# Optimization experiments

Hardware: AMD Instinct MI355X
Metric: run time of the kernel (lower is better)

The kernel has to match this reference:

```python
import jax, jax.numpy as jnp
import numpy as np

N_NODES = 100000
N_EDGES = 1600000


def setup_inputs() -> dict:
    key = jax.random.key(0)
    ks = jax.random.split(key, 8)
    x = jax.random.normal(ks[0], (N_NODES, 100), dtype=jnp.float32)
    edge_index = jax.random.randint(ks[1], (2, N_EDGES), 0, N_NODES, dtype=jnp.int64)
    edge_weight = jax.random.uniform(ks[2], (N_EDGES,), dtype=jnp.float32)
    # params (kaiming-ish scale)
    W_conv = jax.random.normal(ks[3], (100, 32), dtype=jnp.float32) * (1.0 / np.sqrt(100))
    b_conv = jnp.zeros((32,), jnp.float32)
    W1 = jax.random.normal(ks[4], (32, 16), dtype=jnp.float32) * (1.0 / np.sqrt(32))
    b1 = jnp.zeros((16,), jnp.float32)
    W2 = jax.random.normal(ks[5], (16, 8), dtype=jnp.float32) * (1.0 / np.sqrt(16))
    b2 = jnp.zeros((8,), jnp.float32)
    W3 = jax.random.normal(ks[6], (8, 10), dtype=jnp.float32) * (1.0 / np.sqrt(8))
    b3 = jnp.zeros((10,), jnp.float32)
    return {"x": x, "edge_index": edge_index, "edge_weight": edge_weight,
            "W_conv": W_conv, "b_conv": b_conv, "W1": W1, "b1": b1,
            "W2": W2, "b2": b2, "W3": W3, "b3": b3}


def gcn_conv(x, edge_index, W, b, n_nodes):
    # PyG GCNConv: add self-loops, symmetric deg^-0.5 normalization, unit edge weights
    loop = jnp.arange(n_nodes, dtype=edge_index.dtype)
    src = jnp.concatenate([edge_index[0], loop])
    dst = jnp.concatenate([edge_index[1], loop])
    deg = jax.ops.segment_sum(jnp.ones_like(dst, dtype=x.dtype), dst,
                              num_segments=n_nodes)
    dinv = jax.lax.rsqrt(jnp.maximum(deg, 1e-12))  # deg >= 1 due to self-loops
    norm = dinv[src] * dinv[dst]                   # [E+N]
    h = x @ W                                      # [N, 32]
    msg = h[src] * norm[:, None]                   # gather + scale
    out = jax.ops.segment_sum(msg, dst, num_segments=n_nodes)  # scatter-add
    return out + b


def reference(x, edge_index, edge_weight, W_conv, b_conv, W1, b1, W2, b2, W3, b3):
    # edge_weight is accepted by the original forward but never used (conv1(x, edge_index))
    n_nodes = x.shape[0]
    h = jax.nn.relu(gcn_conv(x, edge_index, W_conv, b_conv, n_nodes))
    # F.dropout with training=False (eval) is identity
    h = jax.nn.relu(h @ W1 + b1)
    h = jax.nn.relu(h @ W2 + b2)
    h = h @ W3 + b3
    return jax.nn.log_softmax(h, axis=1)
```

## Files before the change

### kernel.cpp

```cpp
#include <hip/hip_runtime.h>
#include <hip/hip_fp16.h>
#include <math.h>

#define N_NODES 100000
#define N_EDGES 1600000
#define F_IN 100
#define F_H 32

#define BKT_SHIFT 7
#define BKT_C 128
#define NBK 782
#define BKT_CAP 2560

#define BF_B 1024
#define BF_EPT 8
#define BF_TILE 8192
#define BF_GRID 196

#define XW_ROWS 256
#define XW_S2 51
#define XW_NT 391

#define FUSE_GRID 512
#define SM_BYTES 58624

#define AG_B 512
#define AG_CAP BKT_CAP
#define AG_EPT 5

__global__ __launch_bounds__(BF_B) void fused1_kernel(
        const int* __restrict__ src, const int* __restrict__ dst,
        int* __restrict__ gcursor, int* __restrict__ xwctr,
        unsigned* __restrict__ packed,
        const float* __restrict__ x, const float* __restrict__ W,
        float* __restrict__ h2f) {
    __shared__ char smraw[SM_BYTES] __attribute__((aligned(16)));
    __shared__ int stile;
    int t = threadIdx.x;
    if (blockIdx.x < BF_GRID) {
        int* cnt = (int*)smraw;
        int* lbase = cnt + NBK;
        int* gbase = lbase + NBK;
        int* wsums = gbase + NBK;
        int* ptot = wsums + 16;
        unsigned* stage = (unsigned*)(ptot + 1);
        unsigned short* stageB = (unsigned short*)(stage + BF_TILE);
        long base = (long)blockIdx.x * BF_TILE;
        for (int i = t; i < NBK; i += BF_B) cnt[i] = 0;
        __syncthreads();
        int myb[BF_EPT]; int mypos[BF_EPT]; unsigned mypk[BF_EPT];
#pragma unroll
        for (int k = 0; k < BF_EPT; k++) {
            long e = base + t + (long)k * BF_B;
            myb[k] = -1;
            if (e < N_EDGES) {
                int d = dst[e];
                int sI = src[e];
                int b = d >> BKT_SHIFT;
                myb[k] = b;
                mypk[k] = (unsigned)sI | ((unsigned)(d & (BKT_C - 1)) << 17);
                mypos[k] = atomicAdd(&cnt[b], 1);
            }
        }
        __syncthreads();
        if (t < NBK && cnt[t] > 0)
            gbase[t] = t * BKT_CAP + atomicAdd(&gcursor[t], cnt[t]);
        int lane = t & 63, w = t >> 6;
        int v = (t < NBK) ? cnt[t] : 0;
        int sc = v;
#pragma unroll
        for (int off = 1; off < 64; off <<= 1) {
            int xx = __shfl_up(sc, off, 64);
            if (lane >= off) sc += xx;
        }
        if (lane == 63) wsums[w] = sc;
        __syncthreads();
        int pre = 0;
#pragma unroll
        for (int u = 0; u < 16; u++) pre += (u < w) ? wsums[u] : 0;
        int incl = sc + pre;
        if (t < NBK) lbase[t] = incl - v;
        if (t == BF_B - 1) ptot[0] = incl;
        __syncthreads();
#pragma unroll
        for (int k = 0; k < BF_EPT; k++) {
            if (myb[k] >= 0) {
                int p = lbase[myb[k]] + mypos[k];
                stage[p] = mypk[k];
                stageB[p] = (unsigned short)myb[k];
            }
        }
        __syncthreads();
        int T = ptot[0];
        for (int i = t; i < T; i += BF_B) {
            int b = stageB[i];
            packed[gbase[b] + (i - lbase[b])] = stage[i];
        }
    }
    __half2* xs = (__half2*)smraw;
    for (;;) {
        if (t == 0) stile = atomicAdd(xwctr, 1);
        __syncthreads();
        int tb = stile;
        if (tb >= XW_NT) break;
        int rbase = tb * XW_ROWS;
        int rows = min(XW_ROWS, N_NODES - rbase);
        int total = rows * F_IN;
        const float4* gx4 = (const float4*)(x + (long)rbase * F_IN);
        for (int i4 = t; i4 < (total >> 2); i4 += BF_B) {
            float4 v = gx4[i4];
            int i = i4 << 2;
            int r = i / F_IN;
            int k = i - r * F_IN;
            __half2* p = xs + r * XW_S2 + (k >> 1);
            p[0] = __floats2half2_rn(v.x, v.y);
            p[1] = __floats2half2_rn(v.z, v.w);
        }
        __syncthreads();
        int r = t & (XW_ROWS - 1);
        int colbase = __builtin_amdgcn_readfirstlane((t >> 8) << 3);
        if (r < rows) {
            const float* Wp = W + colbase;
            float acc[8];
#pragma unroll
            for (int j = 0; j < 8; j++) acc[j] = 0.f;
            const __half2* xr = xs + r * XW_S2;
#pragma unroll 5
            for (int k2 = 0; k2 < F_IN / 2; k2++) {
                float2 xv = __half22float2(xr[k2]);
#pragma unroll
                for (int j = 0; j < 8; j++)
                    acc[j] = fmaf(xv.y, Wp[(2 * k2 + 1) * F_H + j],
                                  fmaf(xv.x, Wp[(2 * k2) * F_H + j], acc[j]));
            }
            float4* dst4 = (float4*)(h2f + (long)(rbase + r) * F_H + colbase);
            dst4[0] = make_float4(acc[0], acc[1], acc[2], acc[3]);
            dst4[1] = make_float4(acc[4], acc[5], acc[6], acc[7]);
        }
        __syncthreads();
    }
}

__global__ __launch_bounds__(256) void scale_kernel(
        const int* __restrict__ blen, const unsigned* __restrict__ packed,
        const float* __restrict__ h2f, __half* __restrict__ h2) {
    __shared__ int cnt[BKT_C];
    __shared__ float sdv[BKT_C];
    int t = threadIdx.x;
    int b = blockIdx.x;
    if (t < BKT_C) cnt[t] = 0;
    __syncthreads();
    int beg = b * BKT_CAP, end = beg + blen[b];
    for (int i = beg + t; i < end; i += 256)
        atomicAdd(&cnt[(packed[i] >> 17) & (BKT_C - 1)], 1);
    __syncthreads();
    if (t < BKT_C) sdv[t] = rsqrtf((float)cnt[t] + 1.0f);
    __syncthreads();
    int rbase = b << BKT_SHIFT;
    int rows = min(BKT_C, N_NODES - rbase);
    const float4* src4 = (const float4*)(h2f + (long)rbase * F_H);
    float2* dst2 = (float2*)h2;
    for (int i4 = t; i4 < rows * 8; i4 += 256) {
        float4 v = src4[i4];
        float dv = sdv[i4 >> 3];
        float2 o;
        __half2* oh = (__half2*)&o;
        oh[0] = __floats2half2_rn(v.x * dv, v.y * dv);
        oh[1] = __floats2half2_rn(v.z * dv, v.w * dv);
        dst2[(long)rbase * 8 + i4] = o;
    }
}

__global__ __launch_bounds__(AG_B) void agg_kernel(
        const int* __restrict__ blen, const unsigned* __restrict__ packed,
        const __half* __restrict__ h2,
        const float* __restrict__ bc,
        const float* __restrict__ W1, const float* __restrict__ b1,
        const float* __restrict__ W2, const float* __restrict__ b2,
        const float* __restrict__ W3, const float* __restrict__ b3,
        float* __restrict__ out) {
    __shared__ float accL[BKT_C * 33];
    __shared__ int esrc[AG_CAP];
    __shared__ int cnt[BKT_C];
    __shared__ int lbase[BKT_C];
    __shared__ int wsum;
    __shared__ float sbc[32], sW1[512], sb1[16], sW2[128], sb2[8], sW3[80], sb3[10];
    int t = threadIdx.x;
    if (t < 32) sbc[t] = bc[t];
    if (t < 512) sW1[t] = W1[t];
    if (t < 16) sb1[t] = b1[t];
    if (t < 128) sW2[t] = W2[t];
    if (t < 8) sb2[t] = b2[t];
    if (t < 80) sW3[t] = W3[t];
    if (t < 10) sb3[t] = b3[t];

    int b = blockIdx.x;
    int beg = b * BKT_CAP;
    int cnum = blen[b];
    if (t < BKT_C) cnt[t] = 0;
    __syncthreads();
    unsigned pk[AG_EPT]; int pos[AG_EPT];
#pragma unroll
    for (int k = 0; k < AG_EPT; k++) {
        int idx = t + k * AG_B;
        pk[k] = 0xFFFFFFFFu;
        if (idx < cnum) {
            unsigned p = packed[beg + idx];
            pk[k] = p;
            pos[k] = atomicAdd(&cnt[(p >> 17) & (BKT_C - 1)], 1);
        }
    }
    __syncthreads();
    {
        int lane = t & 63;
        int v = 0;
        if (t < BKT_C) {
            v = cnt[t];
#pragma unroll
            for (int off = 1; off < 64; off <<= 1) {
                int xx = __shfl_up(v, off, 64);
                if (lane >= off) v += xx;
            }
            if (t == 63) wsum = v;
        }
        __syncthreads();
        if (t < BKT_C) {
            if (t >= 64) v += wsum;
            lbase[t] = v;
        }
    }
    __syncthreads();
#pragma unroll
    for (int k = 0; k < AG_EPT; k++) {
        if (pk[k] != 0xFFFFFFFFu) {
            int lid = (pk[k] >> 17) & (BKT_C - 1);
            esrc[lbase[lid] - cnt[lid] + pos[k]] = (int)(pk[k] & 0x1FFFF);
        }
    }
    __syncthreads();
    {
        int g = t >> 2, l = t & 3;
        const float4* h2o = (const float4*)h2;
        int e = lbase[g] - cnt[g];
        int eend = lbase[g];
        float a0 = 0.f, a1 = 0.f, a2 = 0.f, a3 = 0.f;
        float a4 = 0.f, a5 = 0.f, a6 = 0.f, a7 = 0.f;
        for (; e + 8 <= eend; e += 8) {
            int s0 = esrc[e], s1 = esrc[e+1], s2 = esrc[e+2], s3 = esrc[e+3];
            int s4 = esrc[e+4], s5 = esrc[e+5], s6 = esrc[e+6], s7 = esrc[e+7];
            float4 q0 = h2o[s0 * 4 + l];
            float4 q1 = h2o[s1 * 4 + l];
            float4 q2 = h2o[s2 * 4 + l];
            float4 q3 = h2o[s3 * 4 + l];
            float4 q4 = h2o[s4 * 4 + l];
            float4 q5 = h2o[s5 * 4 + l];
            float4 q6 = h2o[s6 * 4 + l];
            float4 q7 = h2o[s7 * 4 + l];
#pragma unroll
            for (int u = 0; u < 8; u++) {
                float4 q = (u == 0) ? q0 : (u == 1) ? q1 : (u == 2) ? q2 :
                           (u == 3) ? q3 : (u == 4) ? q4 : (u == 5) ? q5 :
                           (u == 6) ? q6 : q7;
                const __half2* hp = (const __half2*)&q;
                float2 f0 = __half22float2(hp[0]);
                float2 f1 = __half22float2(hp[1]);
                float2 f2 = __half22float2(hp[2]);
                float2 f3 = __half22float2(hp[3]);
                a0 += f0.x; a1 += f0.y; a2 += f1.x; a3 += f1.y;
                a4 += f2.x; a5 += f2.y; a6 += f3.x; a7 += f3.y;
            }
        }
        for (; e < eend; e++) {
            float4 q = h2o[esrc[e] * 4 + l];
            const __half2* hp = (const __half2*)&q;
            float2 f0 = __half22float2(hp[0]);
            float2 f1 = __half22float2(hp[1]);
            float2 f2 = __half22float2(hp[2]);
            float2 f3 = __half22float2(hp[3]);
            a0 += f0.x; a1 += f0.y; a2 += f1.x; a3 += f1.y;
            a4 += f2.x; a5 += f2.y; a6 += f3.x; a7 += f3.y;
        }
        float* ap = accL + g * 33 + 8 * l;
        ap[0] = a0; ap[1] = a1; ap[2] = a2; ap[3] = a3;
        ap[4] = a4; ap[5] = a5; ap[6] = a6; ap[7] = a7;
    }
    __syncthreads();

    int n = (b << BKT_SHIFT) + t;
    if (t < BKT_C && n < N_NODES) {
        float dv = rsqrtf((float)cnt[t] + 1.0f);
        const __half2* h2v = (const __half2*)h2;
        float a[32];
#pragma unroll
        for (int q = 0; q < 16; q++) {
            float2 hv = __half22float2(h2v[n * 16 + q]);
            a[2*q]   = fmaxf((accL[t * 33 + 2*q]   + hv.x) * dv + sbc[2*q],   0.f);
            a[2*q+1] = fmaxf((accL[t * 33 + 2*q+1] + hv.y) * dv + sbc[2*q+1], 0.f);
        }
        float t1[16];
#pragma unroll
        for (int j = 0; j < 16; j++) {
            float s = sb1[j];
            for (int k = 0; k < 32; k++) s += a[k] * sW1[k * 16 + j];
            t1[j] = fmaxf(s, 0.f);
        }
        float t2[8];
#pragma unroll
        for (int j = 0; j < 8; j++) {
            float s = sb2[j];
            for (int k = 0; k < 16; k++) s += t1[k] * sW2[k * 8 + j];
            t2[j] = fmaxf(s, 0.f);
        }
        float t3[10];
#pragma unroll
        for (int j = 0; j < 10; j++) {
            float s = sb3[j];
            for (int k = 0; k < 8; k++) s += t2[k] * sW3[k * 10 + j];
            t3[j] = s;
        }
        float m = t3[0];
#pragma unroll
        for (int j = 1; j < 10; j++) m = fmaxf(m, t3[j]);
        float se = 0.f;
#pragma unroll
        for (int j = 0; j < 10; j++) se += expf(t3[j] - m);
        float lse = logf(se) + m;
        float* op = out + (long)n * 10;
#pragma unroll
        for (int j = 0; j < 10; j++) op[j] = t3[j] - lse;
    }
}

extern "C" void kernel_launch(void* const* d_in, const int* in_sizes, int n_in,
                              void* d_out, int out_size, void* d_ws, size_t ws_size,
                              hipStream_t stream) {
    const float* x  = (const float*)d_in[0];
    const int*   ei = (const int*)d_in[1];
    const float* Wc = (const float*)d_in[3];
    const float* bc = (const float*)d_in[4];
    const float* W1 = (const float*)d_in[5];
    const float* b1 = (const float*)d_in[6];
    const float* W2 = (const float*)d_in[7];
    const float* b2 = (const float*)d_in[8];
    const float* W3 = (const float*)d_in[9];
    const float* b3 = (const float*)d_in[10];
    float* out = (float*)d_out;

    __half*   h2      = (__half*)d_ws;
    unsigned* packed  = (unsigned*)((char*)d_ws + (long)N_NODES * F_H * 2);
    float*    h2f     = (float*)(packed + (long)NBK * BKT_CAP);
    int*      gcursor = (int*)(h2f + (long)N_NODES * F_H);
    int*      xwctr   = gcursor + NBK;

    const int* srcp = ei;
    const int* dstp = ei + N_EDGES;

    hipMemsetAsync(gcursor, 0, (NBK + 1) * sizeof(int), stream);
    fused1_kernel<<<FUSE_GRID, BF_B, 0, stream>>>(srcp, dstp, gcursor, xwctr,
                                                  packed, x, Wc, h2f);
    scale_kernel<<<NBK, 256, 0, stream>>>(gcursor, packed, h2f, h2);
    agg_kernel<<<NBK, AG_B, 0, stream>>>(gcursor, packed, h2, bc, W1, b1,
                                         W2, b2, W3, b3, out);
}
```

Before: 171.6 us.

## Split fp16 node features into two planes and gather each plane separately

The scaled fp16 feature table is stored as two planar halves, features 0-15 and 16-31, each 32 bytes per node, instead of one 64-byte row. The aggregation kernel then gathers neighbors in two passes, one per plane, using 8-byte loads. Each pass touches a table half the size, so the intent is better cache hit rates for the random gathers. In exchange it doubles the number of gather instructions and re-reads the edge list from shared memory.

```diff
diff --git a/kernel.cpp b/kernel.cpp
--- a/kernel.cpp
+++ b/kernel.cpp
@@ -27,6 +27,9 @@
 #define AG_B 512
 #define AG_CAP BKT_CAP
 #define AG_EPT 5
+
+#define PL_H2   ((long)N_NODES * 8)
+#define PL_F2   ((long)N_NODES * 4)
 
 __global__ __launch_bounds__(BF_B) void fused1_kernel(
         const int* __restrict__ src, const int* __restrict__ dst,
@@ -162,12 +165,15 @@
     float2* dst2 = (float2*)h2;
     for (int i4 = t; i4 < rows * 8; i4 += 256) {
         float4 v = src4[i4];
-        float dv = sdv[i4 >> 3];
+        int r = i4 >> 3;
+        int q = i4 & 7;
+        float dv = sdv[r];
         float2 o;
         __half2* oh = (__half2*)&o;
         oh[0] = __floats2half2_rn(v.x * dv, v.y * dv);
         oh[1] = __floats2half2_rn(v.z * dv, v.w * dv);
-        dst2[(long)rbase * 8 + i4] = o;
+        long n = rbase + r;
+        dst2[(q >= 4 ? PL_F2 : 0) + n * 4 + (q & 3)] = o;
     }
 }
 
@@ -240,49 +246,76 @@
     __syncthreads();
     {
         int g = t >> 2, l = t & 3;
-        const float4* h2o = (const float4*)h2;
-        int e = lbase[g] - cnt[g];
+        const float2* p0 = (const float2*)h2;
+        const float2* p1 = p0 + PL_F2;
+        int e0 = lbase[g] - cnt[g];
         int eend = lbase[g];
         float a0 = 0.f, a1 = 0.f, a2 = 0.f, a3 = 0.f;
-        float a4 = 0.f, a5 = 0.f, a6 = 0.f, a7 = 0.f;
+        float b0 = 0.f, b1v = 0.f, b2v = 0.f, b3v = 0.f;
+        int e = e0;
         for (; e + 8 <= eend; e += 8) {
             int s0 = esrc[e], s1 = esrc[e+1], s2 = esrc[e+2], s3 = esrc[e+3];
             int s4 = esrc[e+4], s5 = esrc[e+5], s6 = esrc[e+6], s7 = esrc[e+7];
-            float4 q0 = h2o[s0 * 4 + l];
-            float4 q1 = h2o[s1 * 4 + l];
-            float4 q2 = h2o[s2 * 4 + l];
-            float4 q3 = h2o[s3 * 4 + l];
-            float4 q4 = h2o[s4 * 4 + l];
-            float4 q5 = h2o[s5 * 4 + l];
-            float4 q6 = h2o[s6 * 4 + l];
-            float4 q7 = h2o[s7 * 4 + l];
+            float2 q0 = p0[(long)s0 * 4 + l];
+            float2 q1 = p0[(long)s1 * 4 + l];
+            float2 q2 = p0[(long)s2 * 4 + l];
+            float2 q3 = p0[(long)s3 * 4 + l];
+            float2 q4 = p0[(long)s4 * 4 + l];
+            float2 q5 = p0[(long)s5 * 4 + l];
+            float2 q6 = p0[(long)s6 * 4 + l];
+            float2 q7 = p0[(long)s7 * 4 + l];
 #pragma unroll
             for (int u = 0; u < 8; u++) {
-                float4 q = (u == 0) ? q0 : (u == 1) ? q1 : (u == 2) ? q2 :
+                float2 q = (u == 0) ? q0 : (u == 1) ? q1 : (u == 2) ? q2 :
                            (u == 3) ? q3 : (u == 4) ? q4 : (u == 5) ? q5 :
                            (u == 6) ? q6 : q7;
                 const __half2* hp = (const __half2*)&q;
                 float2 f0 = __half22float2(hp[0]);
                 float2 f1 = __half22float2(hp[1]);
-                float2 f2 = __half22float2(hp[2]);
-                float2 f3 = __half22float2(hp[3]);
                 a0 += f0.x; a1 += f0.y; a2 += f1.x; a3 += f1.y;
-                a4 += f2.x; a5 += f2.y; a6 += f3.x; a7 += f3.y;
             }
         }
         for (; e < eend; e++) {
-            float4 q = h2o[esrc[e] * 4 + l];
+            float2 q = p0[(long)esrc[e] * 4 + l];
             const __half2* hp = (const __half2*)&q;
             float2 f0 = __half22float2(hp[0]);
             float2 f1 = __half22float2(hp[1]);
-            float2 f2 = __half22float2(hp[2]);
-            float2 f3 = __half22float2(hp[3]);
             a0 += f0.x; a1 += f0.y; a2 += f1.x; a3 += f1.y;
-            a4 += f2.x; a5 += f2.y; a6 += f3.x; a7 += f3.y;
-        }
-        float* ap = accL + g * 33 + 8 * l;
-        ap[0] = a0; ap[1] = a1; ap[2] = a2; ap[3] = a3;
-        ap[4] = a4; ap[5] = a5; ap[6] = a6; ap[7] = a7;
+        }
+        e = e0;
+        for (; e + 8 <= eend; e += 8) {
+            int s0 = esrc[e], s1 = esrc[e+1], s2 = esrc[e+2], s3 = esrc[e+3];
+            int s4 = esrc[e+4], s5 = esrc[e+5], s6 = esrc[e+6], s7 = esrc[e+7];
+            float2 q0 = p1[(long)s0 * 4 + l];
+            float2 q1 = p1[(long)s1 * 4 + l];
+            float2 q2 = p1[(long)s2 * 4 + l];
+            float2 q3 = p1[(long)s3 * 4 + l];
+            float2 q4 = p1[(long)s4 * 4 + l];
+            float2 q5 = p1[(long)s5 * 4 + l];
+            float2 q6 = p1[(long)s6 * 4 + l];
+            float2 q7 = p1[(long)s7 * 4 + l];
+#pragma unroll
+            for (int u = 0; u < 8; u++) {
+                float2 q = (u == 0) ? q0 : (u == 1) ? q1 : (u == 2) ? q2 :
+                           (u == 3) ? q3 : (u == 4) ? q4 : (u == 5) ? q5 :
+                           (u == 6) ? q6 : q7;
+                const __half2* hp = (const __half2*)&q;
+                float2 f0 = __half22float2(hp[0]);
+                float2 f1 = __half22float2(hp[1]);
+                b0 += f0.x; b1v += f0.y; b2v += f1.x; b3v += f1.y;
+            }
+        }
+        for (; e < eend; e++) {
+            float2 q = p1[(long)esrc[e] * 4 + l];
+            const __half2* hp = (const __half2*)&q;
+            float2 f0 = __half22float2(hp[0]);
+            float2 f1 = __half22float2(hp[1]);
+            b0 += f0.x; b1v += f0.y; b2v += f1.x; b3v += f1.y;
+        }
+        float* ap = accL + g * 33;
+        ap[4*l+0] = a0;  ap[4*l+1] = a1;  ap[4*l+2] = a2;  ap[4*l+3] = a3;
+        ap[16+4*l+0] = b0; ap[16+4*l+1] = b1v;
+        ap[16+4*l+2] = b2v; ap[16+4*l+3] = b3v;
     }
     __syncthreads();
 
@@ -293,7 +326,8 @@
         float a[32];
 #pragma unroll
         for (int q = 0; q < 16; q++) {
-            float2 hv = __half22float2(h2v[n * 16 + q]);
+            float2 hv = __half22float2(
+                h2v[(q >= 8 ? PL_H2 : 0) + (long)n * 8 + (q & 7)]);
             a[2*q]   = fmaxf((accL[t * 33 + 2*q]   + hv.x) * dv + sbc[2*q],   0.f);
             a[2*q+1] = fmaxf((accL[t * 33 + 2*q+1] + hv.y) * dv + sbc[2*q+1], 0.f);
         }
```

Result: slower. 178.8 us (+4.2%).
